# Kernel tuning notes

Hardware: AMD Instinct MI355X
Metric: run time of the kernel (lower is better)

Reference implementation:

```python
import jax, jax.numpy as jnp
import numpy as np

NBITS = 16  # posit word size passed to posit_forward
ES = 1      # posit exponent-field size (standard posit16 uses es=1)


def posit_quant(x, nbits=NBITS, es=ES):
    """Round-trip float -> posit(nbits, es) -> float, vectorized.

    Emulates posit quantization: regime length determines how many fraction
    bits remain, mantissa is rounded to that precision, magnitude clamped to
    [minpos, maxpos]. Straight-through estimator keeps gradients useful.
    """
    absx = jnp.abs(x)
    sign = jnp.sign(x)
    safe = jnp.maximum(absx, 1e-30)
    scale = jnp.floor(jnp.log2(safe))                 # binary exponent
    useed_log2 = float(2 ** es)
    regime = jnp.floor(scale / useed_log2)
    rlen = jnp.where(regime >= 0, regime + 2.0, 1.0 - regime)  # regime bits
    fbits = jnp.clip(nbits - 1 - es - rlen, 0.0, 28.0)          # fraction bits left
    pw = jnp.exp2(fbits)
    m = safe * jnp.exp2(-scale)                       # mantissa in [1, 2)
    mq = 1.0 + jnp.round((m - 1.0) * pw) / pw
    maxscale = float((nbits - 2) * (2 ** es))         # maxpos = 2^((n-2)*2^es)
    mag = jnp.clip(mq * jnp.exp2(scale), jnp.exp2(-maxscale), jnp.exp2(maxscale))
    q = jnp.where(absx == 0.0, 0.0, sign * mag)
    return x + jax.lax.stop_gradient(q - x)           # straight-through


def posit_linear(x, W, b):
    # posit_forward: quantize operands, GEMM, quantize the accumulated output
    xq = posit_quant(x)
    Wq = posit_quant(W)
    bq = posit_quant(b)
    return posit_quant(xq @ Wq.T + bq)


def setup_inputs() -> dict:
    key = jax.random.key(0)
    ks = jax.random.split(key, 7)

    def w(k, o, i):
        return jax.random.normal(k, (o, i), jnp.float32) * (1.0 / np.sqrt(i))

    return {
        "x": jax.random.normal(ks[0], (4096, 2048), jnp.float32),
        "W0": w(ks[1], 8192, 2048),
        "b0": jax.random.normal(ks[2], (8192,), jnp.float32) * 0.01,
        "W1": w(ks[3], 8192, 8192),
        "b1": jax.random.normal(ks[4], (8192,), jnp.float32) * 0.01,
        "W2": w(ks[5], 2048, 8192),
        "b2": jax.random.normal(ks[6], (2048,), jnp.float32) * 0.01,
    }


def reference(x, W0, b0, W1, b1, W2, b2):
    # layer 0: posit linear + relu (clamp(min=0))
    h = jax.nn.relu(posit_linear(x, W0, b0))
    # layer 1: posit linear + relu
    h = jax.nn.relu(posit_linear(h, W1, b1))
    # layer 2: posit linear, identity activation
    return posit_linear(h, W2, b2)
```

## Files before the change

### kernel.cpp

```cpp
#include <hip/hip_runtime.h>
#include <hip/hip_bf16.h>
#include <cstdint>
#include <cstddef>

using bf16 = __hip_bfloat16;
typedef __attribute__((ext_vector_type(8))) short short8;
typedef __attribute__((ext_vector_type(4))) float f32x4;

__device__ __forceinline__ float posit_quant_f32(float x) {
  float absx = fabsf(x);
  float safe = fmaxf(absx, 1e-30f);
  uint32_t bits = __float_as_uint(safe);
  int scale = (int)((bits >> 23) & 0xFFu) - 127;
  int regime = scale >> 1;
  int rlen = (regime >= 0) ? (regime + 2) : (1 - regime);
  int fbits = 14 - rlen;
  fbits = fbits < 0 ? 0 : fbits;
  float pw = (float)(1 << fbits);
  float m = __uint_as_float((bits & 0x007FFFFFu) | 0x3F800000u);
  float mq = rintf((m - 1.0f) * pw) * (1.0f / pw) + 1.0f;
  float mag = mq * __uint_as_float((uint32_t)(scale + 127) << 23);
  mag = fminf(fmaxf(mag, 0x1p-28f), 0x1p28f);
  return (absx == 0.0f) ? 0.0f : copysignf(mag, x);
}

__device__ __forceinline__ ushort4 pq_bf16x4(float4 v) {
  ushort4 o;
  o.x = __builtin_bit_cast(unsigned short, __float2bfloat16(posit_quant_f32(v.x)));
  o.y = __builtin_bit_cast(unsigned short, __float2bfloat16(posit_quant_f32(v.y)));
  o.z = __builtin_bit_cast(unsigned short, __float2bfloat16(posit_quant_f32(v.z)));
  o.w = __builtin_bit_cast(unsigned short, __float2bfloat16(posit_quant_f32(v.w)));
  return o;
}

__global__ void kquant_all(const float* __restrict__ s0, bf16* __restrict__ d0,
                           const float* __restrict__ s1, bf16* __restrict__ d1,
                           const float* __restrict__ s2, bf16* __restrict__ d2,
                           const float* __restrict__ s3, bf16* __restrict__ d3,
                           long c0, long c1, long c2, long c3) {
  long i = (long)blockIdx.x * blockDim.x + threadIdx.x;
  long stride = (long)gridDim.x * blockDim.x;
  for (; i < c3; i += stride) {
    const float* s; bf16* d; long j;
    if (i < c0)      { s = s0; d = d0; j = i; }
    else if (i < c1) { s = s1; d = d1; j = i - c0; }
    else if (i < c2) { s = s2; d = d2; j = i - c1; }
    else             { s = s3; d = d3; j = i - c2; }
    float4 v = ((const float4*)s)[j];
    ((ushort4*)d)[j] = pq_bf16x4(v);
  }
}

__global__ void kcombine(const float* __restrict__ p, const float* __restrict__ bias,
                         float* __restrict__ out, long n4, long halfn, int cmask) {
  long i = (long)blockIdx.x * blockDim.x + threadIdx.x;
  long stride = (long)gridDim.x * blockDim.x;
  for (; i < n4; i += stride) {
    float4 a = ((const float4*)p)[i];
    float4 b = ((const float4*)(p + halfn))[i];
    int c0 = (int)(i & cmask) * 4;
    float4 o;
    o.x = posit_quant_f32(a.x + b.x + posit_quant_f32(bias[c0 + 0]));
    o.y = posit_quant_f32(a.y + b.y + posit_quant_f32(bias[c0 + 1]));
    o.z = posit_quant_f32(a.z + b.z + posit_quant_f32(bias[c0 + 2]));
    o.w = posit_quant_f32(a.w + b.w + posit_quant_f32(bias[c0 + 3]));
    ((float4*)out)[i] = o;
  }
}

typedef __attribute__((address_space(1))) uint32_t gu32;
typedef __attribute__((address_space(3))) uint32_t lu32;

#define SBAR()  do { __builtin_amdgcn_sched_barrier(0); __builtin_amdgcn_s_barrier(); \
                     __builtin_amdgcn_sched_barrier(0); } while (0)
#define LGKM0() do { asm volatile("s_waitcnt lgkmcnt(0)" ::: "memory"); \
                     __builtin_amdgcn_sched_barrier(0); } while (0)
#define VMCNT(N) asm volatile("s_waitcnt vmcnt(" #N ")" ::: "memory")

#define AB0 0
#define AB1 32768
#define BB0 65536
#define BB1 98304

#define STG(SRC, KT, H, DST) do { \
    const char* _s = (SRC) + (long)((H) * 128) * Kb + (long)(KT) * 128; \
    char* _d = smem + (DST) + (H) * 16384 + wave * 1024; \
    __builtin_amdgcn_global_load_lds((const gu32*)_s, (lu32*)_d, 16, 0, 0); \
    __builtin_amdgcn_global_load_lds((const gu32*)(_s + 64 * Kb), (lu32*)(_d + 8192), 16, 0, 0); \
  } while (0)

#define LDA8(AOFF, FI, CK) (*(const short8*)(smem + (AOFF) + aRel + (FI) * 2048 + (CK)))
#define LDB8(BOFF, FJ, CK) (*(const short8*)(smem + (BOFF) + bRel + (FJ) * 2048 + (CK)))

#define MQ(FI0, FJ0) do { \
    _Pragma("unroll") \
    for (int fi = 0; fi < 4; ++fi) { \
      _Pragma("unroll") \
      for (int fj = 0; fj < 2; ++fj) { \
        acc[(FI0) + fi][(FJ0) + fj] = __builtin_amdgcn_mfma_f32_16x16x32_bf16( \
            afr[fi][0], bfr[(FJ0) + fj][0], acc[(FI0) + fi][(FJ0) + fj], 0, 0, 0); \
        acc[(FI0) + fi][(FJ0) + fj] = __builtin_amdgcn_mfma_f32_16x16x32_bf16( \
            afr[fi][1], bfr[(FJ0) + fj][1], acc[(FI0) + fi][(FJ0) + fj], 0, 0, 0); \
      } \
    } \
  } while (0)

template <int MODE>
__global__ __launch_bounds__(512, 2) void gemm256_posit(
    const bf16* __restrict__ A, const bf16* __restrict__ B,
    const float* __restrict__ bias, void* __restrict__ out,
    int M, int N, int Kfull, int Kloop, int nbt, int cpx) {
  __shared__ __align__(1024) char smem[131072];

  const int tid  = threadIdx.x;
  const int lane = tid & 63;
  const int wave = tid >> 6;
  const int wr = wave >> 2;
  const int wc = wave & 3;

  const int flat = blockIdx.x;
  const int wgid = (flat & 7) * cpx + (flat >> 3);
  const int split = wgid / nbt;
  const int t = wgid - split * nbt;
  const int nbx = N >> 8;
  const long brow0 = (long)(t / nbx) * 256;
  const long bcol0 = (long)(t % nbx) * 256;

  const long Kb = (long)Kfull * 2;
  const long splitoff = (long)split * Kloop * 2;

  const int srow = tid >> 3;
  const int scb  = ((tid & 7) * 16) ^ (((tid >> 3) & 7) << 4);
  const char* srcA = (const char*)A + (brow0 + srow) * Kb + scb + splitoff;
  const char* srcB = (const char*)B + (bcol0 + srow) * Kb + scb + splitoff;

  const int fr  = lane & 15;
  const int swz = (lane & 7) << 4;
  const int ck0 = (((lane >> 4) << 4)) ^ swz;
  const int ck1 = (64 + ((lane >> 4) << 4)) ^ swz;
  const int aRel = wr * 16384 + fr * 128;
  const int bRel = wc * 8192 + fr * 128;

  f32x4 acc[8][4] = {};
  short8 afr[4][2], bfr[4][2];

  const int nkt = Kloop >> 6;
  const int np  = nkt >> 1;

  STG(srcB, 0, 0, BB0); STG(srcB, 0, 1, BB0);
  STG(srcA, 0, 0, AB0); STG(srcA, 0, 1, AB0);
  STG(srcB, 1, 0, BB1); STG(srcB, 1, 1, BB1);
  VMCNT(4);
  SBAR();

#pragma unroll 1
  for (int i = 0; i < np; ++i) {
    const int kA1 = 2 * i + 1;
    const int kS2 = (2 * i + 2) & (nkt - 1);
    const int kS3 = (2 * i + 3) & (nkt - 1);

#pragma unroll
    for (int f = 0; f < 4; ++f) { afr[f][0] = LDA8(AB0, f, ck0); afr[f][1] = LDA8(AB0, f, ck1); }
#pragma unroll
    for (int f = 0; f < 2; ++f) { bfr[f][0] = LDB8(BB0, f, ck0); bfr[f][1] = LDB8(BB0, f, ck1); }
    STG(srcA, kA1, 0, AB1);
    SBAR(); LGKM0();
    __builtin_amdgcn_s_setprio(1); MQ(0, 0); __builtin_amdgcn_s_setprio(0);
    SBAR();

#pragma unroll
    for (int f = 2; f < 4; ++f) { bfr[f][0] = LDB8(BB0, f, ck0); bfr[f][1] = LDB8(BB0, f, ck1); }
    STG(srcA, kA1, 1, AB1);
    SBAR(); LGKM0();
    __builtin_amdgcn_s_setprio(1); MQ(0, 2); __builtin_amdgcn_s_setprio(0);
    SBAR();

#pragma unroll
    for (int f = 0; f < 4; ++f) { afr[f][0] = LDA8(AB0, f + 4, ck0); afr[f][1] = LDA8(AB0, f + 4, ck1); }
    STG(srcB, kS2, 0, BB0);
    SBAR(); LGKM0();
    __builtin_amdgcn_s_setprio(1); MQ(4, 0); __builtin_amdgcn_s_setprio(0);
    SBAR();

    STG(srcB, kS2, 1, BB0);
    VMCNT(4);
    SBAR();
    __builtin_amdgcn_s_setprio(1); MQ(4, 2); __builtin_amdgcn_s_setprio(0);
    SBAR();

#pragma unroll
    for (int f = 0; f < 4; ++f) { afr[f][0] = LDA8(AB1, f, ck0); afr[f][1] = LDA8(AB1, f, ck1); }
#pragma unroll
    for (int f = 0; f < 2; ++f) { bfr[f][0] = LDB8(BB1, f, ck0); bfr[f][1] = LDB8(BB1, f, ck1); }
    STG(srcA, kS2, 0, AB0);
    SBAR(); LGKM0();
    __builtin_amdgcn_s_setprio(1); MQ(0, 0); __builtin_amdgcn_s_setprio(0);
    SBAR();

#pragma unroll
    for (int f = 2; f < 4; ++f) { bfr[f][0] = LDB8(BB1, f, ck0); bfr[f][1] = LDB8(BB1, f, ck1); }
    STG(srcA, kS2, 1, AB0);
    SBAR(); LGKM0();
    __builtin_amdgcn_s_setprio(1); MQ(0, 2); __builtin_amdgcn_s_setprio(0);
    SBAR();

#pragma unroll
    for (int f = 0; f < 4; ++f) { afr[f][0] = LDA8(AB1, f + 4, ck0); afr[f][1] = LDA8(AB1, f + 4, ck1); }
    STG(srcB, kS3, 0, BB1);
    SBAR(); LGKM0();
    __builtin_amdgcn_s_setprio(1); MQ(4, 0); __builtin_amdgcn_s_setprio(0);
    SBAR();

    STG(srcB, kS3, 1, BB1);
    VMCNT(4);
    SBAR();
    __builtin_amdgcn_s_setprio(1); MQ(4, 2); __builtin_amdgcn_s_setprio(0);
    SBAR();
  }
  asm volatile("s_waitcnt vmcnt(0)" ::: "memory");

  const int orow = (lane >> 4) * 4;
  const long row0 = brow0 + wr * 128;
  const long col0 = bcol0 + wc * 64;
  const long obase = (MODE == 2) ? (long)split * M * N : 0;
#pragma unroll
  for (int fj = 0; fj < 4; ++fj) {
    const long col = col0 + fj * 16 + fr;
    const float bv = (MODE == 2) ? 0.0f : posit_quant_f32(bias[col]);
#pragma unroll
    for (int fi = 0; fi < 8; ++fi) {
#pragma unroll
      for (int q = 0; q < 4; ++q) {
        float v = acc[fi][fj][q];
        if (MODE != 2) {
          v = posit_quant_f32(v + bv);
          if (MODE == 0) v = fmaxf(v, 0.0f);
        }
        const long idx = obase + (row0 + fi * 16 + orow + q) * (long)N + col;
        if (MODE == 0) ((bf16*)out)[idx] = __float2bfloat16(v);
        else           ((float*)out)[idx] = v;
      }
    }
  }
}

#define GBM 128
#define GBN 128
#define GBK 32

__device__ __forceinline__ void gload_lds16(const void* g, void* l) {
  __builtin_amdgcn_global_load_lds((const gu32*)g, (lu32*)l, 16, 0, 0);
}

template <bool RELU, bool OUTBF16>
__global__ __launch_bounds__(256, 2) void gemm_bt_posit(
    const bf16* __restrict__ A, const bf16* __restrict__ B,
    const float* __restrict__ bias, void* __restrict__ out,
    int M, int N, int K) {
  __shared__ __align__(1024) bf16 sA[GBM][GBK];
  __shared__ __align__(1024) bf16 sB[GBN][GBK];

  const int tid = threadIdx.x;
  const int lane = tid & 63;
  const int wave = tid >> 6;
  const int wr = wave >> 1;
  const int wc = wave & 1;
  const long brow0 = (long)blockIdx.y * GBM;
  const long bcol0 = (long)blockIdx.x * GBN;

  const int srow = lane >> 2;
  const int scol = (lane & 3) * 8;
  const int seg0 = wave * 2;

  const bf16* gA0 = A + (brow0 + seg0 * 16 + srow) * (long)K + scol;
  const bf16* gA1 = A + (brow0 + seg0 * 16 + 16 + srow) * (long)K + scol;
  const bf16* gB0 = B + (bcol0 + seg0 * 16 + srow) * (long)K + scol;
  const bf16* gB1 = B + (bcol0 + seg0 * 16 + 16 + srow) * (long)K + scol;
  bf16* lA0 = (bf16*)sA + seg0 * 512;
  bf16* lA1 = lA0 + 512;
  bf16* lB0 = (bf16*)sB + seg0 * 512;
  bf16* lB1 = lB0 + 512;

  f32x4 acc[4][4] = {};
  const int fr = lane & 15;
  const int fk = (lane >> 4) * 8;

  for (int kt = 0; kt < K; kt += GBK) {
    __syncthreads();
    gload_lds16(gA0 + kt, lA0);
    gload_lds16(gA1 + kt, lA1);
    gload_lds16(gB0 + kt, lB0);
    gload_lds16(gB1 + kt, lB1);
    __syncthreads();

    short8 af[4], bfv[4];
#pragma unroll
    for (int i = 0; i < 4; ++i) af[i] = *(const short8*)&sA[wr * 64 + i * 16 + fr][fk];
#pragma unroll
    for (int j = 0; j < 4; ++j) bfv[j] = *(const short8*)&sB[wc * 64 + j * 16 + fr][fk];
#pragma unroll
    for (int i = 0; i < 4; ++i)
#pragma unroll
      for (int j = 0; j < 4; ++j)
        acc[i][j] = __builtin_amdgcn_mfma_f32_16x16x32_bf16(af[i], bfv[j], acc[i][j], 0, 0, 0);
  }

  const int orow = (lane >> 4) * 4;
  const long row0 = brow0 + wr * 64;
  const long col0 = bcol0 + wc * 64;
#pragma unroll
  for (int j = 0; j < 4; ++j) {
    const long col = col0 + j * 16 + fr;
    const float bv = posit_quant_f32(bias[col]);
#pragma unroll
    for (int i = 0; i < 4; ++i) {
#pragma unroll
      for (int q = 0; q < 4; ++q) {
        float v = posit_quant_f32(acc[i][j][q] + bv);
        if (RELU) v = fmaxf(v, 0.0f);
        const long idx = (row0 + i * 16 + orow + q) * (long)N + col;
        if (OUTBF16) ((bf16*)out)[idx] = __float2bfloat16(v);
        else         ((float*)out)[idx] = v;
      }
    }
  }
}

extern "C" void kernel_launch(void* const* d_in, const int* in_sizes, int n_in,
                              void* d_out, int out_size, void* d_ws, size_t ws_size,
                              hipStream_t stream) {
  const float* x  = (const float*)d_in[0];
  const float* W0 = (const float*)d_in[1];
  const float* b0 = (const float*)d_in[2];
  const float* W1 = (const float*)d_in[3];
  const float* b1 = (const float*)d_in[4];
  const float* W2 = (const float*)d_in[5];
  const float* b2 = (const float*)d_in[6];

  const int M = 4096, D0 = 2048, D1 = 8192, D2 = 8192, DO = 2048;

  char* ws = (char*)d_ws;
  size_t off = 0;
  auto alloc = [&](size_t bytes) {
    char* p = ws + off;
    off += (bytes + 255) & ~(size_t)255;
    return p;
  };
  bf16* xq  = (bf16*)alloc((size_t)M * D0 * 2);
  bf16* W0q = (bf16*)alloc((size_t)D1 * D0 * 2);
  bf16* W1q = (bf16*)alloc((size_t)D2 * D1 * 2);
  bf16* W2q = (bf16*)alloc((size_t)DO * D2 * 2);
  bf16* h0  = (bf16*)alloc((size_t)M * D1 * 2);
  bf16* h1  = (bf16*)alloc((size_t)M * D2 * 2);
  float* part = (float*)alloc((size_t)2 * M * DO * 4);
  const bool splitk = (off <= ws_size);
  (void)in_sizes; (void)n_in; (void)out_size;

  {
    long q0 = (long)M * D0 / 4;
    long q1 = q0 + (long)D1 * D0 / 4;
    long q2 = q1 + (long)D2 * D1 / 4;
    long q3 = q2 + (long)DO * D2 / 4;
    kquant_all<<<2048, 256, 0, stream>>>(x, xq, W0, W0q, W1, W1q, W2, W2q,
                                         q0, q1, q2, q3);
  }

  {
    int nbt = (D1 / 256) * (M / 256), nwg = nbt;
    gemm256_posit<0><<<dim3(nwg), dim3(512), 0, stream>>>(
        xq, W0q, b0, h0, M, D1, D0, D0, nbt, nwg / 8);
  }
  {
    int nbt = (D2 / 256) * (M / 256), nwg = nbt;
    gemm256_posit<0><<<dim3(nwg), dim3(512), 0, stream>>>(
        h0, W1q, b1, h1, M, D2, D1, D1, nbt, nwg / 8);
  }
  if (splitk) {
    int nbt = (DO / 256) * (M / 256);
    int nwg = nbt * 2;
    gemm256_posit<2><<<dim3(nwg), dim3(512), 0, stream>>>(
        h1, W2q, nullptr, part, M, DO, D2, D2 / 2, nbt, nwg / 8);
    long n4 = (long)M * DO / 4;
    kcombine<<<2048, 256, 0, stream>>>(part, b2, (float*)d_out, n4,
                                       (long)M * DO, DO / 4 - 1);
  } else {
    gemm_bt_posit<false, false><<<dim3(DO / GBN, M / GBM), dim3(256), 0, stream>>>(
        h1, W2q, b2, (float*)d_out, M, DO, D2);
  }
}
```

Before: 888.5 us.

## Software-pipeline LDS fragment loads one phase ahead of MFMA blocks

Restructures the GEMM main loop so that shared-memory fragment reads for the next MFMA phase are issued right after the current MFMA group, before the barrier, rather than just before use with an explicit lgkmcnt(0) wait. This is meant to hide LDS read latency behind MFMA execution and remove the per-phase full LDS wait. B fragments are split into separate b01/b23 registers, so the compiler's implicit waits now cover dependencies. The risks are added register pressure under launch bounds (512, 2) and LDS reads crossing barriers, which relies on buffer reuse ordering remaining correct.

```diff
diff --git a/kernel.cpp b/kernel.cpp
--- a/kernel.cpp
+++ b/kernel.cpp
@@ -73,8 +73,6 @@
 
 #define SBAR()  do { __builtin_amdgcn_sched_barrier(0); __builtin_amdgcn_s_barrier(); \
                      __builtin_amdgcn_sched_barrier(0); } while (0)
-#define LGKM0() do { asm volatile("s_waitcnt lgkmcnt(0)" ::: "memory"); \
-                     __builtin_amdgcn_sched_barrier(0); } while (0)
 #define VMCNT(N) asm volatile("s_waitcnt vmcnt(" #N ")" ::: "memory")
 
 #define AB0 0
@@ -92,15 +90,28 @@
 #define LDA8(AOFF, FI, CK) (*(const short8*)(smem + (AOFF) + aRel + (FI) * 2048 + (CK)))
 #define LDB8(BOFF, FJ, CK) (*(const short8*)(smem + (BOFF) + bRel + (FJ) * 2048 + (CK)))
 
-#define MQ(FI0, FJ0) do { \
+#define PREF_ALO(BUF) do { _Pragma("unroll") \
+    for (int f = 0; f < 4; ++f) { ar[f][0] = LDA8(BUF, f, ck0); ar[f][1] = LDA8(BUF, f, ck1); } \
+  } while (0)
+#define PREF_AHI(BUF) do { _Pragma("unroll") \
+    for (int f = 0; f < 4; ++f) { ar[f][0] = LDA8(BUF, f + 4, ck0); ar[f][1] = LDA8(BUF, f + 4, ck1); } \
+  } while (0)
+#define PREF_B01(BUF) do { _Pragma("unroll") \
+    for (int f = 0; f < 2; ++f) { b01[f][0] = LDB8(BUF, f, ck0); b01[f][1] = LDB8(BUF, f, ck1); } \
+  } while (0)
+#define PREF_B23(BUF) do { _Pragma("unroll") \
+    for (int f = 0; f < 2; ++f) { b23[f][0] = LDB8(BUF, f + 2, ck0); b23[f][1] = LDB8(BUF, f + 2, ck1); } \
+  } while (0)
+
+#define MQS(ACC0, BS, FJ0) do { \
     _Pragma("unroll") \
     for (int fi = 0; fi < 4; ++fi) { \
       _Pragma("unroll") \
       for (int fj = 0; fj < 2; ++fj) { \
-        acc[(FI0) + fi][(FJ0) + fj] = __builtin_amdgcn_mfma_f32_16x16x32_bf16( \
-            afr[fi][0], bfr[(FJ0) + fj][0], acc[(FI0) + fi][(FJ0) + fj], 0, 0, 0); \
-        acc[(FI0) + fi][(FJ0) + fj] = __builtin_amdgcn_mfma_f32_16x16x32_bf16( \
-            afr[fi][1], bfr[(FJ0) + fj][1], acc[(FI0) + fi][(FJ0) + fj], 0, 0, 0); \
+        acc[(ACC0) + fi][(FJ0) + fj] = __builtin_amdgcn_mfma_f32_16x16x32_bf16( \
+            ar[fi][0], BS[fj][0], acc[(ACC0) + fi][(FJ0) + fj], 0, 0, 0); \
+        acc[(ACC0) + fi][(FJ0) + fj] = __builtin_amdgcn_mfma_f32_16x16x32_bf16( \
+            ar[fi][1], BS[fj][1], acc[(ACC0) + fi][(FJ0) + fj], 0, 0, 0); \
       } \
     } \
   } while (0)
@@ -142,7 +153,7 @@
   const int bRel = wc * 8192 + fr * 128;
 
   f32x4 acc[8][4] = {};
-  short8 afr[4][2], bfr[4][2];
+  short8 ar[4][2], b01[2][2], b23[2][2];
 
   const int nkt = Kloop >> 6;
   const int np  = nkt >> 1;
@@ -152,6 +163,8 @@
   STG(srcB, 1, 0, BB1); STG(srcB, 1, 1, BB1);
   VMCNT(4);
   SBAR();
+  PREF_ALO(AB0); PREF_B01(BB0);
+  __builtin_amdgcn_sched_barrier(0);
 
 #pragma unroll 1
   for (int i = 0; i < np; ++i) {
@@ -159,65 +172,55 @@
     const int kS2 = (2 * i + 2) & (nkt - 1);
     const int kS3 = (2 * i + 3) & (nkt - 1);
 
-#pragma unroll
-    for (int f = 0; f < 4; ++f) { afr[f][0] = LDA8(AB0, f, ck0); afr[f][1] = LDA8(AB0, f, ck1); }
-#pragma unroll
-    for (int f = 0; f < 2; ++f) { bfr[f][0] = LDB8(BB0, f, ck0); bfr[f][1] = LDB8(BB0, f, ck1); }
+    PREF_B23(BB0);
     STG(srcA, kA1, 0, AB1);
-    SBAR(); LGKM0();
-    __builtin_amdgcn_s_setprio(1); MQ(0, 0); __builtin_amdgcn_s_setprio(0);
-    SBAR();
-
-#pragma unroll
-    for (int f = 2; f < 4; ++f) { bfr[f][0] = LDB8(BB0, f, ck0); bfr[f][1] = LDB8(BB0, f, ck1); }
+    SBAR();
+    __builtin_amdgcn_s_setprio(1); MQS(0, b01, 0); __builtin_amdgcn_s_setprio(0);
+    SBAR();
+
     STG(srcA, kA1, 1, AB1);
-    SBAR(); LGKM0();
-    __builtin_amdgcn_s_setprio(1); MQ(0, 2); __builtin_amdgcn_s_setprio(0);
-    SBAR();
-
-#pragma unroll
-    for (int f = 0; f < 4; ++f) { afr[f][0] = LDA8(AB0, f + 4, ck0); afr[f][1] = LDA8(AB0, f + 4, ck1); }
+    SBAR();
+    __builtin_amdgcn_s_setprio(1); MQS(0, b23, 2); __builtin_amdgcn_s_setprio(0);
+    PREF_AHI(AB0);
+    SBAR();
+
     STG(srcB, kS2, 0, BB0);
-    SBAR(); LGKM0();
-    __builtin_amdgcn_s_setprio(1); MQ(4, 0); __builtin_amdgcn_s_setprio(0);
+    SBAR();
+    __builtin_amdgcn_s_setprio(1); MQS(4, b01, 0); __builtin_amdgcn_s_setprio(0);
     SBAR();
 
     STG(srcB, kS2, 1, BB0);
     VMCNT(4);
     SBAR();
-    __builtin_amdgcn_s_setprio(1); MQ(4, 2); __builtin_amdgcn_s_setprio(0);
-    SBAR();
-
-#pragma unroll
-    for (int f = 0; f < 4; ++f) { afr[f][0] = LDA8(AB1, f, ck0); afr[f][1] = LDA8(AB1, f, ck1); }
-#pragma unroll
-    for (int f = 0; f < 2; ++f) { bfr[f][0] = LDB8(BB1, f, ck0); bfr[f][1] = LDB8(BB1, f, ck1); }
+    __builtin_amdgcn_s_setprio(1); MQS(4, b23, 2); __builtin_amdgcn_s_setprio(0);
+    PREF_ALO(AB1); PREF_B01(BB1);
+    SBAR();
+
+    PREF_B23(BB1);
     STG(srcA, kS2, 0, AB0);
-    SBAR(); LGKM0();
-    __builtin_amdgcn_s_setprio(1); MQ(0, 0); __builtin_amdgcn_s_setprio(0);
-    SBAR();
-
-#pragma unroll
-    for (int f = 2; f < 4; ++f) { bfr[f][0] = LDB8(BB1, f, ck0); bfr[f][1] = LDB8(BB1, f, ck1); }
+    SBAR();
+    __builtin_amdgcn_s_setprio(1); MQS(0, b01, 0); __builtin_amdgcn_s_setprio(0);
+    SBAR();
+
     STG(srcA, kS2, 1, AB0);
-    SBAR(); LGKM0();
-    __builtin_amdgcn_s_setprio(1); MQ(0, 2); __builtin_amdgcn_s_setprio(0);
-    SBAR();
-
-#pragma unroll
-    for (int f = 0; f < 4; ++f) { afr[f][0] = LDA8(AB1, f + 4, ck0); afr[f][1] = LDA8(AB1, f + 4, ck1); }
+    SBAR();
+    __builtin_amdgcn_s_setprio(1); MQS(0, b23, 2); __builtin_amdgcn_s_setprio(0);
+    PREF_AHI(AB1);
+    SBAR();
+
     STG(srcB, kS3, 0, BB1);
-    SBAR(); LGKM0();
-    __builtin_amdgcn_s_setprio(1); MQ(4, 0); __builtin_amdgcn_s_setprio(0);
+    SBAR();
+    __builtin_amdgcn_s_setprio(1); MQS(4, b01, 0); __builtin_amdgcn_s_setprio(0);
     SBAR();
 
     STG(srcB, kS3, 1, BB1);
     VMCNT(4);
     SBAR();
-    __builtin_amdgcn_s_setprio(1); MQ(4, 2); __builtin_amdgcn_s_setprio(0);
-    SBAR();
-  }
-  asm volatile("s_waitcnt vmcnt(0)" ::: "memory");
+    __builtin_amdgcn_s_setprio(1); MQS(4, b23, 2); __builtin_amdgcn_s_setprio(0);
+    PREF_ALO(AB0); PREF_B01(BB0);
+    SBAR();
+  }
+  asm volatile("s_waitcnt vmcnt(0) lgkmcnt(0)" ::: "memory");
 
   const int orow = (lane >> 4) * 4;
   const long row0 = brow0 + wr * 128;
```

Result: no change. 874.8 us (-1.5%).
